# Optimization experiments

Hardware: AMD Instinct MI355X
Metric: run time of the kernel (lower is better)

The kernel has to match this reference:

```python
import jax, jax.numpy as jnp
import numpy as np

H = 1024  # hidden size
IN = 5    # input feature size
OUT = 9   # output classes


def setup_inputs() -> dict:
    key = jax.random.key(0)
    ks = jax.random.split(key, 7)
    s_ih = 1.0 / np.sqrt(H)
    inp = {
        "x": jax.random.normal(ks[0], (2048, 1, IN), dtype=jnp.float32),
        # PyTorch nn.LSTM params, gate order [i, f, g, o] along first axis
        "w_ih": jax.random.uniform(ks[1], (4 * H, IN), jnp.float32, -s_ih, s_ih),
        "w_hh": jax.random.uniform(ks[2], (4 * H, H), jnp.float32, -s_ih, s_ih),
        "b_ih": jax.random.uniform(ks[3], (4 * H,), jnp.float32, -s_ih, s_ih),
        "b_hh": jax.random.uniform(ks[4], (4 * H,), jnp.float32, -s_ih, s_ih),
        # nn.Linear(H, OUT)
        "w_out": jax.random.uniform(ks[5], (OUT, H), jnp.float32, -s_ih, s_ih),
        "b_out": jax.random.uniform(ks[6], (OUT,), jnp.float32, -s_ih, s_ih),
    }
    return inp


def _lstm_last_h(x, w_ih, w_hh, b_ih, b_hh):
    # x: [T, 1, IN] (batch=1). Precompute input contributions for all steps.
    T = x.shape[0]
    x2 = x.reshape(T, IN)
    gates_x = x2 @ w_ih.T + (b_ih + b_hh)  # [T, 4H]

    def step(carry, gx):
        h, c = carry
        g = gx + w_hh @ h  # [4H]
        i = jax.nn.sigmoid(g[:H])
        f = jax.nn.sigmoid(g[H:2 * H])
        gc = jnp.tanh(g[2 * H:3 * H])
        o = jax.nn.sigmoid(g[3 * H:])
        c = f * c + i * gc
        h = o * jnp.tanh(c)
        return (h, c), None

    h0 = jnp.zeros((H,), x.dtype)
    c0 = jnp.zeros((H,), x.dtype)
    (h_last, _), _ = jax.lax.scan(step, (h0, c0), gates_x)
    return h_last  # [H]


def reference(x, w_ih, w_hh, b_ih, b_hh, w_out, b_out):
    h_last = _lstm_last_h(x, w_ih, w_hh, b_ih, b_hh)
    z = jnp.tanh(h_last)                       # F.tanh(lstm_out)
    logits = z @ w_out.T + b_out               # [OUT]
    out = jax.nn.log_softmax(logits, axis=-1)  # dim=1 over classes
    return out.reshape(1, OUT)                 # [1, 9] like torch
```

## Files before the change

### kernel.cpp

```cpp
#include <hip/hip_runtime.h>
#include <math.h>


typedef unsigned int u32;
typedef unsigned long long u64;

constexpr int kH     = 1024;
constexpr int kT     = 2048;
constexpr int kIN    = 5;
constexpr int kOUT   = 9;
constexpr int kNWG   = 64;
constexpr int kBLOCK = 512;
constexpr int kAtoms = 512;

__device__ __forceinline__ float sigm_(float v) {
  return 1.0f / (1.0f + expf(-v));
}
__device__ __forceinline__ float tanh_(float v) {
  return 1.0f - 2.0f / (expf(2.0f * v) + 1.0f);
}
__device__ __forceinline__ u32 bf16_rne(float f) {
  u32 b = __float_as_uint(f);
  return (b + 0x7FFFu + ((b >> 16) & 1u)) >> 16;
}
__device__ __forceinline__ float lo_f(u32 p) { return __uint_as_float(p << 16); }
__device__ __forceinline__ float hi_f(u32 p) { return __uint_as_float(p & 0xFFFF0000u); }

__device__ __forceinline__ u64 poll1(const u64* p) {
  u64 a;
  asm volatile(
      "global_load_dwordx2 %0, %1, off sc0 sc1\n\t"
      "s_waitcnt vmcnt(0)"
      : "=v"(a) : "v"(p) : "memory");
  return a;
}

__device__ __forceinline__ void poll8(const u64* p, u64& a0, u64& a1, u64& a2,
                                      u64& a3, u64& a4, u64& a5, u64& a6,
                                      u64& a7) {
  asm volatile(
      "global_load_dwordx2 %0, %8, off sc0 sc1\n\t"
      "global_load_dwordx2 %1, %8, off offset:512 sc0 sc1\n\t"
      "global_load_dwordx2 %2, %8, off offset:1024 sc0 sc1\n\t"
      "global_load_dwordx2 %3, %8, off offset:1536 sc0 sc1\n\t"
      "global_load_dwordx2 %4, %8, off offset:2048 sc0 sc1\n\t"
      "global_load_dwordx2 %5, %8, off offset:2560 sc0 sc1\n\t"
      "global_load_dwordx2 %6, %8, off offset:3072 sc0 sc1\n\t"
      "global_load_dwordx2 %7, %8, off offset:3584 sc0 sc1\n\t"
      "s_waitcnt vmcnt(0)"
      : "=&v"(a0), "=&v"(a1), "=&v"(a2), "=&v"(a3),
        "=&v"(a4), "=&v"(a5), "=&v"(a6), "=&v"(a7)
      : "v"(p)
      : "memory");
}

__global__ __launch_bounds__(kBLOCK, 2) void lstm_v8(
    const float* __restrict__ x,
    const float* __restrict__ w_ih,
    const float* __restrict__ w_hh,
    const float* __restrict__ b_ih,
    const float* __restrict__ b_hh,
    const float* __restrict__ w_out,
    const float* __restrict__ b_out,
    float* __restrict__ out,
    u64* __restrict__ ring) {
  const int pid  = blockIdx.x;
  const int tid  = threadIdx.x;
  const int w    = tid >> 6;
  const int lane = tid & 63;

  __shared__ float x_lds[kT * kIN];
  __shared__ float h_lds[kH];
  __shared__ float pacc[2][7][64];
  __shared__ int   gcnt;

  for (int i = tid; i < kT * kIN; i += kBLOCK) x_lds[i] = x[i];
  if (tid == 0) gcnt = 0;

  const int grow = (lane >> 4) * kH + pid * 16 + (lane & 15);
  const int cb   = 128 * w;

  float wreg[128];
  {
    const float* sp = w_hh + (size_t)grow * kH + cb;
#pragma unroll
    for (int m = 0; m < 128; m += 4) {
      const float4 v4 = *(const float4*)(sp + m);
      wreg[m] = v4.x; wreg[m + 1] = v4.y; wreg[m + 2] = v4.z; wreg[m + 3] = v4.w;
    }
  }
  float wihr[kIN];
#pragma unroll
  for (int k = 0; k < kIN; ++k) wihr[k] = w_ih[grow * kIN + k];
  const float biasr = b_ih[grow] + b_hh[grow];

  float cst = 0.0f;
  __syncthreads();

  for (int t = 0; t < kT; ++t) {
    float gx = biasr;
#pragma unroll
    for (int k = 0; k < kIN; ++k) gx = fmaf(wihr[k], x_lds[t * kIN + k], gx);

    const u64* pb = ring + (size_t)(t & 3) * kAtoms + 64 * w + lane;
    u64 a;
    do {
      a = poll1(pb);
    } while (!__all((u32)(a >> 32) == (u32)t));

    const u32 d = (u32)a;
    *(float2*)&h_lds[cb + 2 * lane] = make_float2(lo_f(d), hi_f(d));

    float acc0 = 0.0f, acc1 = 0.0f, acc2 = 0.0f, acc3 = 0.0f;
#pragma unroll
    for (int m = 0; m < 128; m += 4) {
      acc0 = fmaf(wreg[m + 0], h_lds[cb + m + 0], acc0);
      acc1 = fmaf(wreg[m + 1], h_lds[cb + m + 1], acc1);
      acc2 = fmaf(wreg[m + 2], h_lds[cb + m + 2], acc2);
      acc3 = fmaf(wreg[m + 3], h_lds[cb + m + 3], acc3);
    }
    const float part = (acc0 + acc1) + (acc2 + acc3);

    if (w < 7) {
      pacc[t & 1][w][lane] = part;
      if (lane == 0)
        __hip_atomic_fetch_add(&gcnt, 1, __ATOMIC_RELEASE,
                               __HIP_MEMORY_SCOPE_WORKGROUP);
    } else {
      while (__hip_atomic_load(&gcnt, __ATOMIC_ACQUIRE,
                               __HIP_MEMORY_SCOPE_WORKGROUP) < 7 * (t + 1)) { }
      float gtot = part + gx;
#pragma unroll
      for (int w2 = 0; w2 < 7; ++w2) gtot += pacc[t & 1][w2][lane];

      const int gate = lane >> 4;
      const float u = (gate == 2) ? 2.0f * gtot : gtot;
      float n = sigm_(u);
      n = (gate == 2) ? (2.0f * n - 1.0f) : n;

      const int j = lane & 15;
      const float ni = __shfl(n, j);
      const float nf = __shfl(n, 16 + j);
      const float ng = __shfl(n, 32 + j);
      const float no = __shfl(n, 48 + j);
      cst = nf * cst + ni * ng;
      const float hval = no * tanh_(cst);

      const float ph0 = __shfl(hval, 2 * lane);
      const float ph1 = __shfl(hval, 2 * lane + 1);
      if (lane < 8) {
        const u64 atom = ((u64)(u32)(t + 1) << 32) |
                         (u64)(bf16_rne(ph0) | (bf16_rne(ph1) << 16));
        __hip_atomic_store(ring + (size_t)((t + 1) & 3) * kAtoms + pid * 8 + lane,
                           atom, __ATOMIC_RELAXED, __HIP_MEMORY_SCOPE_AGENT);
      }
    }
  }

  if (pid == 0 && w == 0) {
    const u64* pb = ring + (size_t)(kT & 3) * kAtoms + lane;
    u64 a0, a1, a2, a3, a4, a5, a6, a7;
    bool ok;
    do {
      poll8(pb, a0, a1, a2, a3, a4, a5, a6, a7);
      ok = ((u32)(a0 >> 32) == (u32)kT) & ((u32)(a1 >> 32) == (u32)kT) &
           ((u32)(a2 >> 32) == (u32)kT) & ((u32)(a3 >> 32) == (u32)kT) &
           ((u32)(a4 >> 32) == (u32)kT) & ((u32)(a5 >> 32) == (u32)kT) &
           ((u32)(a6 >> 32) == (u32)kT) & ((u32)(a7 >> 32) == (u32)kT);
    } while (!__all(ok));

    u64 av[8] = {a0, a1, a2, a3, a4, a5, a6, a7};
    float logits[kOUT];
#pragma unroll
    for (int r = 0; r < kOUT; ++r) logits[r] = 0.0f;
#pragma unroll
    for (int m = 0; m < 8; ++m) {
      const u32 d = (u32)av[m];
      const float z0 = tanh_(lo_f(d));
      const float z1 = tanh_(hi_f(d));
      const int col = 2 * lane + 128 * m;
#pragma unroll
      for (int r = 0; r < kOUT; ++r) {
        const float2 wv = *(const float2*)(w_out + (size_t)r * kH + col);
        logits[r] = fmaf(wv.x, z0, fmaf(wv.y, z1, logits[r]));
      }
    }
#pragma unroll
    for (int r = 0; r < kOUT; ++r) {
#pragma unroll
      for (int off = 32; off; off >>= 1)
        logits[r] += __shfl_xor(logits[r], off);
      logits[r] += b_out[r];
    }
    if (lane == 0) {
      float m = logits[0];
#pragma unroll
      for (int r = 1; r < kOUT; ++r) m = fmaxf(m, logits[r]);
      float s = 0.0f;
#pragma unroll
      for (int r = 0; r < kOUT; ++r) s += expf(logits[r] - m);
      const float lse = m + logf(s);
#pragma unroll
      for (int r = 0; r < kOUT; ++r) out[r] = logits[r] - lse;
    }
  }
}

extern "C" void kernel_launch(void* const* d_in, const int* in_sizes, int n_in,
                              void* d_out, int out_size, void* d_ws, size_t ws_size,
                              hipStream_t stream) {
  const float* x     = (const float*)d_in[0];
  const float* w_ih  = (const float*)d_in[1];
  const float* w_hh  = (const float*)d_in[2];
  const float* b_ih  = (const float*)d_in[3];
  const float* b_hh  = (const float*)d_in[4];
  const float* w_out = (const float*)d_in[5];
  const float* b_out = (const float*)d_in[6];
  float* out  = (float*)d_out;
  u64*   ring = (u64*)d_ws;

  hipMemsetAsync(d_ws, 0, (size_t)4 * kAtoms * sizeof(u64), stream);

  lstm_v8<<<kNWG, kBLOCK, 0, stream>>>(x, w_ih, w_hh, b_ih, b_hh,
                                       w_out, b_out, out, ring);
}
```

Baseline: 3.771 ms.

## Replicate h broadcast ring across R copies to spread polling contention

Each workgroup now publishes its h slice into R replicated ring copies (R chosen from workspace size, up to 8), and each consumer polls the replica chosen by its pid. This spreads the 64-way polling traffic on the same cache lines across more addresses, cutting contention on the per-step cross-workgroup exchange. It also switches the activations to fast __expf/__fdividef intrinsics and vectorizes the h LDS reads to float4. The trade-offs are more publishing stores per step, a larger memset, and slightly less accurate sigmoid/tanh.

```diff
diff --git a/kernel.cpp b/kernel.cpp
--- a/kernel.cpp
+++ b/kernel.cpp
@@ -11,13 +11,12 @@
 constexpr int kOUT   = 9;
 constexpr int kNWG   = 64;
 constexpr int kBLOCK = 512;
-constexpr int kAtoms = 512;
 
 __device__ __forceinline__ float sigm_(float v) {
-  return 1.0f / (1.0f + expf(-v));
+  return __fdividef(1.0f, 1.0f + __expf(-v));
 }
 __device__ __forceinline__ float tanh_(float v) {
-  return 1.0f - 2.0f / (expf(2.0f * v) + 1.0f);
+  return 1.0f - __fdividef(2.0f, __expf(2.0f * v) + 1.0f);
 }
 __device__ __forceinline__ u32 bf16_rne(float f) {
   u32 b = __float_as_uint(f);
@@ -54,7 +53,7 @@
       : "memory");
 }
 
-__global__ __launch_bounds__(kBLOCK, 2) void lstm_v8(
+__global__ __launch_bounds__(kBLOCK, 2) void lstm_v9(
     const float* __restrict__ x,
     const float* __restrict__ w_ih,
     const float* __restrict__ w_hh,
@@ -63,14 +62,17 @@
     const float* __restrict__ w_out,
     const float* __restrict__ b_out,
     float* __restrict__ out,
-    u64* __restrict__ ring) {
+    u64* __restrict__ ring,
+    u32 slotStride,
+    u32 repMask,
+    u32 pubLanes) {
   const int pid  = blockIdx.x;
   const int tid  = threadIdx.x;
   const int w    = tid >> 6;
   const int lane = tid & 63;
 
   __shared__ float x_lds[kT * kIN];
-  __shared__ float h_lds[kH];
+  __shared__ __align__(16) float h_lds[kH];
   __shared__ float pacc[2][7][64];
   __shared__ int   gcnt;
 
@@ -94,6 +96,7 @@
   for (int k = 0; k < kIN; ++k) wihr[k] = w_ih[grow * kIN + k];
   const float biasr = b_ih[grow] + b_hh[grow];
 
+  const u32 myRep = (u32)pid & repMask;
   float cst = 0.0f;
   __syncthreads();
 
@@ -102,7 +105,8 @@
 #pragma unroll
     for (int k = 0; k < kIN; ++k) gx = fmaf(wihr[k], x_lds[t * kIN + k], gx);
 
-    const u64* pb = ring + (size_t)(t & 3) * kAtoms + 64 * w + lane;
+    const u64* pb = ring + (size_t)(t & 3) * slotStride + myRep * 512 +
+                    64 * w + lane;
     u64 a;
     do {
       a = poll1(pb);
@@ -114,10 +118,11 @@
     float acc0 = 0.0f, acc1 = 0.0f, acc2 = 0.0f, acc3 = 0.0f;
 #pragma unroll
     for (int m = 0; m < 128; m += 4) {
-      acc0 = fmaf(wreg[m + 0], h_lds[cb + m + 0], acc0);
-      acc1 = fmaf(wreg[m + 1], h_lds[cb + m + 1], acc1);
-      acc2 = fmaf(wreg[m + 2], h_lds[cb + m + 2], acc2);
-      acc3 = fmaf(wreg[m + 3], h_lds[cb + m + 3], acc3);
+      const float4 h4 = *(const float4*)&h_lds[cb + m];
+      acc0 = fmaf(wreg[m + 0], h4.x, acc0);
+      acc1 = fmaf(wreg[m + 1], h4.y, acc1);
+      acc2 = fmaf(wreg[m + 2], h4.z, acc2);
+      acc3 = fmaf(wreg[m + 3], h4.w, acc3);
     }
     const float part = (acc0 + acc1) + (acc2 + acc3);
 
@@ -146,19 +151,21 @@
       cst = nf * cst + ni * ng;
       const float hval = no * tanh_(cst);
 
-      const float ph0 = __shfl(hval, 2 * lane);
-      const float ph1 = __shfl(hval, 2 * lane + 1);
-      if (lane < 8) {
+      const int al = lane & 7;
+      const float ph0 = __shfl(hval, 2 * al);
+      const float ph1 = __shfl(hval, 2 * al + 1);
+      if (lane < (int)pubLanes) {
         const u64 atom = ((u64)(u32)(t + 1) << 32) |
                          (u64)(bf16_rne(ph0) | (bf16_rne(ph1) << 16));
-        __hip_atomic_store(ring + (size_t)((t + 1) & 3) * kAtoms + pid * 8 + lane,
+        __hip_atomic_store(ring + (size_t)((t + 1) & 3) * slotStride +
+                               (size_t)(lane >> 3) * 512 + pid * 8 + al,
                            atom, __ATOMIC_RELAXED, __HIP_MEMORY_SCOPE_AGENT);
       }
     }
   }
 
   if (pid == 0 && w == 0) {
-    const u64* pb = ring + (size_t)(kT & 3) * kAtoms + lane;
+    const u64* pb = ring + (size_t)(kT & 3) * slotStride + lane;
     u64 a0, a1, a2, a3, a4, a5, a6, a7;
     bool ok;
     do {
@@ -176,8 +183,8 @@
 #pragma unroll
     for (int m = 0; m < 8; ++m) {
       const u32 d = (u32)av[m];
-      const float z0 = tanh_(lo_f(d));
-      const float z1 = tanh_(hi_f(d));
+      const float z0 = tanhf(lo_f(d));
+      const float z1 = tanhf(hi_f(d));
       const int col = 2 * lane + 128 * m;
 #pragma unroll
       for (int r = 0; r < kOUT; ++r) {
@@ -219,8 +226,15 @@
   float* out  = (float*)d_out;
   u64*   ring = (u64*)d_ws;
 
-  hipMemsetAsync(d_ws, 0, (size_t)4 * kAtoms * sizeof(u64), stream);
-
-  lstm_v8<<<kNWG, kBLOCK, 0, stream>>>(x, w_ih, w_hh, b_ih, b_hh,
-                                       w_out, b_out, out, ring);
-}
+  int R = 1;
+  if      (ws_size >= 4ull * 8 * 4096) R = 8;
+  else if (ws_size >= 4ull * 4 * 4096) R = 4;
+  else if (ws_size >= 4ull * 2 * 4096) R = 2;
+  const u32 slotStride = (u32)(R * 512);
+
+  hipMemsetAsync(d_ws, 0, (size_t)4 * slotStride * sizeof(u64), stream);
+
+  lstm_v9<<<kNWG, kBLOCK, 0, stream>>>(x, w_ih, w_hh, b_ih, b_hh,
+                                       w_out, b_out, out, ring,
+                                       slotStride, (u32)(R - 1), (u32)(8 * R));
+}
```

After: 3.785 ms, median of 4. No clear change (+0.4%).
